# Kernel optimization log

Hardware: AMD Instinct MI355X
Metric: run time of the kernel (lower is better)

The kernel has to match this reference:

```python
import jax, jax.numpy as jnp
import numpy as np

DIM = 256
HEADS = 8
DIM_HEAD = 64
INNER = HEADS * DIM_HEAD
NUM_BANDS = 16          # hard-coded in __init__
MAX_FREQ = 16.0         # hard-coded in __init__
NORM_SCALE = 51.0       # hard-coded in __init__
RPE_DIM = (NUM_BANDS * 2 + 1) * 2  # 66


def fourier_encode(x, max_freq, num_bands):
    # x: [...] -> [..., 2*num_bands+1]  (sin bands, cos bands, raw)
    x = x[..., None]
    scales = jnp.linspace(1.0, max_freq / 2.0, num_bands, dtype=x.dtype)
    xs = x * scales * jnp.pi
    return jnp.concatenate([jnp.sin(xs), jnp.cos(xs), x], axis=-1)


def rpe_features(query_pos, key_pos):
    # delta[b,i,j] = key_pos[b,j] - query_pos[b,i]  -> [B,Nq,Nk,2]
    delta = key_pos[:, None, :, :] - query_pos[:, :, None, :]
    dx = delta[..., 0] / NORM_SCALE
    dy = delta[..., 1] / NORM_SCALE
    dx = dx / (1.0 + jnp.abs(dx))
    dy = dy / (1.0 + jnp.abs(dy))
    x_enc = fourier_encode(dx, MAX_FREQ, NUM_BANDS)
    y_enc = fourier_encode(dy, MAX_FREQ, NUM_BANDS)
    return jnp.concatenate([x_enc, y_enc], axis=-1)  # [B,Nq,Nk,RPE_DIM]


def setup_inputs() -> dict:
    key = jax.random.key(0)
    ks = jax.random.split(key, 8)
    B, N = 1, 512
    x = jax.random.normal(ks[0], (B, N, DIM), dtype=jnp.float32)
    positions = jax.random.uniform(ks[1], (B, N, 2), dtype=jnp.float32) * 512.0
    s = 0.02
    Wq = jax.random.normal(ks[2], (DIM, INNER), dtype=jnp.float32) * s
    Wk = jax.random.normal(ks[3], (DIM + RPE_DIM, INNER), dtype=jnp.float32) * s
    Wv = jax.random.normal(ks[4], (DIM, INNER), dtype=jnp.float32) * s
    Wo = jax.random.normal(ks[5], (INNER, DIM), dtype=jnp.float32) * s
    bo = jnp.zeros((DIM,), dtype=jnp.float32)
    return {"x": x, "positions": positions, "Wq": Wq, "Wk": Wk, "Wv": Wv, "Wo": Wo, "bo": bo}


def reference(x, positions, Wq, Wk, Wv, Wo, bo):
    B, N, D = x.shape
    H, d = HEADS, DIM_HEAD
    scale = d ** -0.5

    rpe = rpe_features(positions, positions)          # [B,N,N,R]
    q = (x @ Wq).reshape(B, N, H, d)                  # [B,N,H,d]
    v = (x @ Wv).reshape(B, N, H, d)

    # k_ij = W_k @ concat(x_j, rpe_ij); split Wk to avoid expanding x to [B,N,N,D]
    Wk_x, Wk_r = Wk[:D], Wk[D:]
    k_content = x @ Wk_x                               # [B,N,INNER] (key j part)
    k_rpe = jnp.einsum('bijr,re->bije', rpe, Wk_r)     # [B,N,N,INNER]
    k = (k_content[:, None, :, :] + k_rpe).reshape(B, N, N, H, d)

    scores = jnp.einsum('bihd,bijhd->bhij', q, k) * scale
    attn = jax.nn.softmax(scores, axis=-1)
    out = jnp.einsum('bhij,bjhd->bihd', attn, v).reshape(B, N, H * d)
    return out @ Wo + bo
```

## Files before the change

### kernel.cpp

```cpp
#include <hip/hip_runtime.h>
#include <math.h>

#define NQ      512
#define DMODEL  256
#define DINNER  512
#define NH      8
#define DHEAD   64
#define SCALE   0.125f
#define PI_F    3.14159265358979323846f

#define Q_OFF   0
#define KC_OFF  262144
#define V_OFF   524288
#define QW_OFF  786432
#define SC_OFF  1114112
#define IN_OFF  3211264

__global__ __launch_bounds__(256) void k_proj(
    const float* __restrict__ x, const float* __restrict__ Wq,
    const float* __restrict__ Wk, const float* __restrict__ Wv,
    float* __restrict__ ws)
{
    const int z = blockIdx.z;
    const float* W = (z == 0) ? Wq : (z == 1) ? Wk : Wv;
    float* out = ws + ((z == 0) ? Q_OFF : (z == 1) ? KC_OFF : V_OFF);

    __shared__ alignas(16) float Xs[32][68];
    __shared__ alignas(16) float Bs[32][64];

    const int tx = threadIdx.x, ty = threadIdx.y;
    const int tid = ty * 16 + tx;
    const int row0 = blockIdx.y * 64, col0 = blockIdx.x * 64;

    float acc[4][4] = {};

    for (int k0 = 0; k0 < DMODEL; k0 += 32) {
        {
            const int m = tid >> 2;
            const int kk0 = (tid & 3) * 8;
            const float* src = x + (row0 + m) * DMODEL + k0 + kk0;
            float4 a0 = *(const float4*)(src);
            float4 a1 = *(const float4*)(src + 4);
            Xs[kk0 + 0][m] = a0.x; Xs[kk0 + 1][m] = a0.y;
            Xs[kk0 + 2][m] = a0.z; Xs[kk0 + 3][m] = a0.w;
            Xs[kk0 + 4][m] = a1.x; Xs[kk0 + 5][m] = a1.y;
            Xs[kk0 + 6][m] = a1.z; Xs[kk0 + 7][m] = a1.w;
        }
        {
            const int kk = tid >> 3;
            const int n0 = (tid & 7) * 8;
            const float* src = W + (k0 + kk) * DINNER + col0 + n0;
            *(float4*)&Bs[kk][n0]     = *(const float4*)(src);
            *(float4*)&Bs[kk][n0 + 4] = *(const float4*)(src + 4);
        }
        __syncthreads();
        #pragma unroll
        for (int kk = 0; kk < 32; ++kk) {
            float4 a4 = *(const float4*)&Xs[kk][ty * 4];
            float4 b4 = *(const float4*)&Bs[kk][tx * 4];
            float a[4] = {a4.x, a4.y, a4.z, a4.w};
            float b[4] = {b4.x, b4.y, b4.z, b4.w};
            #pragma unroll
            for (int ia = 0; ia < 4; ++ia)
                #pragma unroll
                for (int ib = 0; ib < 4; ++ib)
                    acc[ia][ib] += a[ia] * b[ib];
        }
        __syncthreads();
    }
    #pragma unroll
    for (int ia = 0; ia < 4; ++ia) {
        float4 o = make_float4(acc[ia][0], acc[ia][1], acc[ia][2], acc[ia][3]);
        *(float4*)&out[(row0 + ty * 4 + ia) * DINNER + col0 + tx * 4] = o;
    }
}

__global__ __launch_bounds__(256) void k_qw(
    const float* __restrict__ Wk, float* __restrict__ ws)
{
    const float* q = ws + Q_OFF;
    float* qW = ws + QW_OFF;
    const int h  = blockIdx.x >> 4;
    const int i0 = (blockIdx.x & 15) * 32;

    __shared__ float WrT[64][67];
    __shared__ alignas(16) float Qs[32][68];
    const int tid = threadIdx.x;

    for (int idx = tid; idx < 66 * 64; idx += 256) {
        int r = idx >> 6, d = idx & 63;
        WrT[d][r] = Wk[(DMODEL + r) * DINNER + h * DHEAD + d];
    }
    for (int idx = tid; idx < 32 * 16; idx += 256) {
        int m = idx >> 4, dq = (idx & 15) * 4;
        *(float4*)&Qs[m][dq] = *(const float4*)&q[(i0 + m) * DINNER + h * DHEAD + dq];
    }
    __syncthreads();

    for (int idx = tid; idx < 32 * 66; idx += 256) {
        int m = idx / 66, r = idx - m * 66;
        float acc = 0.f;
        #pragma unroll
        for (int d0 = 0; d0 < 64; d0 += 4) {
            float4 qf = *(const float4*)&Qs[m][d0];
            acc += qf.x * WrT[d0 + 0][r] + qf.y * WrT[d0 + 1][r]
                 + qf.z * WrT[d0 + 2][r] + qf.w * WrT[d0 + 3][r];
        }
        int slot;
        if      (r < 16)  slot = r * 32 + 0 + h;
        else if (r < 32)  slot = (r - 16) * 32 + 8 + h;
        else if (r == 32) slot = 512 + h;
        else if (r < 49)  slot = (r - 33) * 32 + 16 + h;
        else if (r < 65)  slot = (r - 49) * 32 + 24 + h;
        else              slot = 520 + h;
        qW[(i0 + m) * 528 + slot] = acc * SCALE;
    }
}

__global__ __launch_bounds__(256) void k_content(float* __restrict__ ws)
{
    const float* q  = ws + Q_OFF;
    const float* kc = ws + KC_OFF;
    float* sc = ws + SC_OFF;
    const int h = blockIdx.z;
    const int i0 = blockIdx.y * 64, j0 = blockIdx.x * 64;

    __shared__ alignas(16) float Qs[64][68];
    __shared__ alignas(16) float Ks[64][68];
    const int tx = threadIdx.x, ty = threadIdx.y;
    const int tid = ty * 16 + tx;
    {
        const int m = tid >> 2;
        const int d0 = (tid & 3) * 16;
        const float* qs = q  + (i0 + m) * DINNER + h * DHEAD + d0;
        const float* ks = kc + (j0 + m) * DINNER + h * DHEAD + d0;
        #pragma unroll
        for (int l = 0; l < 16; ++l) {
            Qs[d0 + l][m] = qs[l];
            Ks[d0 + l][m] = ks[l];
        }
    }
    __syncthreads();
    float acc[4][4] = {};
    #pragma unroll 8
    for (int d = 0; d < 64; ++d) {
        float4 a4 = *(const float4*)&Qs[d][ty * 4];
        float4 b4 = *(const float4*)&Ks[d][tx * 4];
        float a[4] = {a4.x, a4.y, a4.z, a4.w};
        float b[4] = {b4.x, b4.y, b4.z, b4.w};
        #pragma unroll
        for (int ia = 0; ia < 4; ++ia)
            #pragma unroll
            for (int ib = 0; ib < 4; ++ib)
                acc[ia][ib] += a[ia] * b[ib];
    }
    #pragma unroll
    for (int ia = 0; ia < 4; ++ia) {
        float4 o = make_float4(acc[ia][0] * SCALE, acc[ia][1] * SCALE,
                               acc[ia][2] * SCALE, acc[ia][3] * SCALE);
        *(float4*)&sc[((h * NQ) + i0 + ty * 4 + ia) * NQ + j0 + tx * 4] = o;
    }
}

__global__ __launch_bounds__(256) void k_rpe_softmax(
    const float* __restrict__ pos, float* __restrict__ ws)
{
    const float* qW = ws + QW_OFF;
    float* sc = ws + SC_OFF;
    const int i = blockIdx.x;
    const int tid = threadIdx.x;

    __shared__ alignas(16) float qw[528];
    __shared__ float pbuf[8][512];
    __shared__ float red[8];

    for (int idx = tid; idx < 528; idx += 256) qw[idx] = qW[i * 528 + idx];
    __syncthreads();

    const float pxi = pos[i * 2 + 0];
    const float pyi = pos[i * 2 + 1];
    const float4* qw4 = (const float4*)qw;

    #pragma unroll
    for (int jj = 0; jj < 2; ++jj) {
        const int j = tid + jj * 256;
        float dxr = (pos[j * 2 + 0] - pxi) * (1.0f / 51.0f);
        float dyr = (pos[j * 2 + 1] - pyi) * (1.0f / 51.0f);
        float dx = dxr / (1.0f + fabsf(dxr));
        float dy = dyr / (1.0f + fabsf(dyr));

        float s[8];
        #pragma unroll
        for (int h = 0; h < 8; ++h) s[h] = sc[((h * NQ) + i) * NQ + j];

        float sx, cx, sy, cy, sxp, cxp, syp, cyp;
        __sincosf(dx * PI_F, &sx, &cx);
        __sincosf(dx * (PI_F * 7.0f / 15.0f), &sxp, &cxp);
        __sincosf(dy * PI_F, &sy, &cy);
        __sincosf(dy * (PI_F * 7.0f / 15.0f), &syp, &cyp);

        #pragma unroll
        for (int b = 0; b < 16; ++b) {
            float4 wsx0 = qw4[b * 8 + 0], wsx1 = qw4[b * 8 + 1];
            float4 wcx0 = qw4[b * 8 + 2], wcx1 = qw4[b * 8 + 3];
            float4 wsy0 = qw4[b * 8 + 4], wsy1 = qw4[b * 8 + 5];
            float4 wcy0 = qw4[b * 8 + 6], wcy1 = qw4[b * 8 + 7];
            s[0] += sx * wsx0.x + cx * wcx0.x + sy * wsy0.x + cy * wcy0.x;
            s[1] += sx * wsx0.y + cx * wcx0.y + sy * wsy0.y + cy * wcy0.y;
            s[2] += sx * wsx0.z + cx * wcx0.z + sy * wsy0.z + cy * wcy0.z;
            s[3] += sx * wsx0.w + cx * wcx0.w + sy * wsy0.w + cy * wcy0.w;
            s[4] += sx * wsx1.x + cx * wcx1.x + sy * wsy1.x + cy * wcy1.x;
            s[5] += sx * wsx1.y + cx * wcx1.y + sy * wsy1.y + cy * wcy1.y;
            s[6] += sx * wsx1.z + cx * wcx1.z + sy * wsy1.z + cy * wcy1.z;
            s[7] += sx * wsx1.w + cx * wcx1.w + sy * wsy1.w + cy * wcy1.w;
            float t;
            t = sx * cxp + cx * sxp; cx = cx * cxp - sx * sxp; sx = t;
            t = sy * cyp + cy * syp; cy = cy * cyp - sy * syp; sy = t;
        }
        {
            float4 wdx0 = qw4[128], wdx1 = qw4[129];
            float4 wdy0 = qw4[130], wdy1 = qw4[131];
            s[0] += dx * wdx0.x + dy * wdy0.x;
            s[1] += dx * wdx0.y + dy * wdy0.y;
            s[2] += dx * wdx0.z + dy * wdy0.z;
            s[3] += dx * wdx0.w + dy * wdy0.w;
            s[4] += dx * wdx1.x + dy * wdy1.x;
            s[5] += dx * wdx1.y + dy * wdy1.y;
            s[6] += dx * wdx1.z + dy * wdy1.z;
            s[7] += dx * wdx1.w + dy * wdy1.w;
        }
        #pragma unroll
        for (int h = 0; h < 8; ++h) pbuf[h][j] = s[h];
    }
    __syncthreads();

    const int wave = tid >> 6, lane = tid & 63;
    for (int h = wave * 2; h < wave * 2 + 2; ++h) {
        float m = -1e30f;
        for (int jj2 = lane; jj2 < 512; jj2 += 64) m = fmaxf(m, pbuf[h][jj2]);
        #pragma unroll
        for (int off = 32; off; off >>= 1) m = fmaxf(m, __shfl_xor(m, off));
        float sum = 0.f;
        for (int jj2 = lane; jj2 < 512; jj2 += 64) {
            float e = __expf(pbuf[h][jj2] - m);
            pbuf[h][jj2] = e;
            sum += e;
        }
        #pragma unroll
        for (int off = 32; off; off >>= 1) sum += __shfl_xor(sum, off);
        if (lane == 0) red[h] = 1.0f / sum;
    }
    __syncthreads();
    #pragma unroll
    for (int h = 0; h < 8; ++h) {
        const float inv = red[h];
        sc[((h * NQ) + i) * NQ + tid]       = pbuf[h][tid] * inv;
        sc[((h * NQ) + i) * NQ + tid + 256] = pbuf[h][tid + 256] * inv;
    }
}

__global__ __launch_bounds__(256) void k_av(float* __restrict__ ws)
{
    const float* attn = ws + SC_OFF;
    const float* v    = ws + V_OFF;
    float* inner      = ws + IN_OFF;
    const int h  = blockIdx.y;
    const int i0 = blockIdx.x * 32;

    __shared__ alignas(16) float As[32][36];
    __shared__ alignas(16) float Vs[32][64];
    const int tx = threadIdx.x, ty = threadIdx.y;
    const int tid = ty * 16 + tx;

    float acc[2][4] = {};
    for (int k0 = 0; k0 < NQ; k0 += 32) {
        {
            const int m = tid >> 3;
            const int kk0 = (tid & 7) * 4;
            float4 a4 = *(const float4*)&attn[((h * NQ) + i0 + m) * NQ + k0 + kk0];
            As[kk0 + 0][m] = a4.x; As[kk0 + 1][m] = a4.y;
            As[kk0 + 2][m] = a4.z; As[kk0 + 3][m] = a4.w;
        }
        {
            const int kk = tid >> 3;
            const int n0 = (tid & 7) * 8;
            const float* src = v + (k0 + kk) * DINNER + h * DHEAD + n0;
            *(float4*)&Vs[kk][n0]     = *(const float4*)(src);
            *(float4*)&Vs[kk][n0 + 4] = *(const float4*)(src + 4);
        }
        __syncthreads();
        #pragma unroll
        for (int kk = 0; kk < 32; ++kk) {
            float2 a2 = *(const float2*)&As[kk][ty * 2];
            float4 b4 = *(const float4*)&Vs[kk][tx * 4];
            float b[4] = {b4.x, b4.y, b4.z, b4.w};
            #pragma unroll
            for (int ib = 0; ib < 4; ++ib) {
                acc[0][ib] += a2.x * b[ib];
                acc[1][ib] += a2.y * b[ib];
            }
        }
        __syncthreads();
    }
    #pragma unroll
    for (int ia = 0; ia < 2; ++ia) {
        float4 o = make_float4(acc[ia][0], acc[ia][1], acc[ia][2], acc[ia][3]);
        *(float4*)&inner[(i0 + ty * 2 + ia) * DINNER + h * DHEAD + tx * 4] = o;
    }
}

__global__ __launch_bounds__(256) void k_out(
    const float* __restrict__ Wo, const float* __restrict__ bo,
    float* __restrict__ ws, float* __restrict__ outp)
{
    const float* inner = ws + IN_OFF;
    const int c0 = blockIdx.x * 32;
    const int i0 = blockIdx.y * 32;

    __shared__ alignas(16) float Xs[32][36];
    __shared__ alignas(16) float Bs[32][32];
    const int tx = threadIdx.x, ty = threadIdx.y;
    const int tid = ty * 16 + tx;

    float acc[2][2] = {};
    for (int k0 = 0; k0 < DINNER; k0 += 32) {
        {
            const int m = tid >> 3;
            const int kk0 = (tid & 7) * 4;
            float4 a4 = *(const float4*)&inner[(i0 + m) * DINNER + k0 + kk0];
            Xs[kk0 + 0][m] = a4.x; Xs[kk0 + 1][m] = a4.y;
            Xs[kk0 + 2][m] = a4.z; Xs[kk0 + 3][m] = a4.w;
        }
        {
            const int kk = tid >> 3;
            const int n0 = (tid & 7) * 4;
            *(float4*)&Bs[kk][n0] = *(const float4*)&Wo[(k0 + kk) * DMODEL + c0 + n0];
        }
        __syncthreads();
        #pragma unroll
        for (int kk = 0; kk < 32; ++kk) {
            float2 a2 = *(const float2*)&Xs[kk][ty * 2];
            float2 b2 = *(const float2*)&Bs[kk][tx * 2];
            acc[0][0] += a2.x * b2.x;
            acc[0][1] += a2.x * b2.y;
            acc[1][0] += a2.y * b2.x;
            acc[1][1] += a2.y * b2.y;
        }
        __syncthreads();
    }
    #pragma unroll
    for (int ia = 0; ia < 2; ++ia) {
        float2 o;
        o.x = acc[ia][0] + bo[c0 + tx * 2 + 0];
        o.y = acc[ia][1] + bo[c0 + tx * 2 + 1];
        *(float2*)&outp[(i0 + ty * 2 + ia) * DMODEL + c0 + tx * 2] = o;
    }
}

extern "C" void kernel_launch(void* const* d_in, const int* in_sizes, int n_in,
                              void* d_out, int out_size, void* d_ws, size_t ws_size,
                              hipStream_t stream)
{
    const float* x   = (const float*)d_in[0];
    const float* pos = (const float*)d_in[1];
    const float* Wq  = (const float*)d_in[2];
    const float* Wk  = (const float*)d_in[3];
    const float* Wv  = (const float*)d_in[4];
    const float* Wo  = (const float*)d_in[5];
    const float* bo  = (const float*)d_in[6];
    float* out = (float*)d_out;
    float* ws  = (float*)d_ws;

    k_proj<<<dim3(8, 8, 3), dim3(16, 16), 0, stream>>>(x, Wq, Wk, Wv, ws);
    k_qw<<<dim3(128), dim3(256), 0, stream>>>(Wk, ws);
    k_content<<<dim3(8, 8, 8), dim3(16, 16), 0, stream>>>(ws);
    k_rpe_softmax<<<dim3(512), dim3(256), 0, stream>>>(pos, ws);
    k_av<<<dim3(16, 8), dim3(16, 16), 0, stream>>>(ws);
    k_out<<<dim3(8, 16), dim3(16, 16), 0, stream>>>(Wo, bo, ws, out);
}
```

Baseline: 166.9 us.

## Fuse content scores, RPE bias, softmax and AV into flash-style attention kernel

```diff
diff --git a/kernel.cpp b/kernel.cpp
--- a/kernel.cpp
+++ b/kernel.cpp
@@ -13,8 +13,7 @@
 #define KC_OFF  262144
 #define V_OFF   524288
 #define QW_OFF  786432
-#define SC_OFF  1114112
-#define IN_OFF  3211264
+#define IN_OFF  1064960
 
 __global__ __launch_bounds__(256) void k_proj(
     const float* __restrict__ x, const float* __restrict__ Wq,
@@ -106,207 +105,173 @@
             acc += qf.x * WrT[d0 + 0][r] + qf.y * WrT[d0 + 1][r]
                  + qf.z * WrT[d0 + 2][r] + qf.w * WrT[d0 + 3][r];
         }
-        int slot;
-        if      (r < 16)  slot = r * 32 + 0 + h;
-        else if (r < 32)  slot = (r - 16) * 32 + 8 + h;
-        else if (r == 32) slot = 512 + h;
-        else if (r < 49)  slot = (r - 33) * 32 + 16 + h;
-        else if (r < 65)  slot = (r - 49) * 32 + 24 + h;
-        else              slot = 520 + h;
-        qW[(i0 + m) * 528 + slot] = acc * SCALE;
-    }
-}
-
-__global__ __launch_bounds__(256) void k_content(float* __restrict__ ws)
+        int p = (r < 32) ? r : (r == 32) ? 64 : (r < 65) ? (r - 1) : 65;
+        qW[(i0 + m) * 544 + h * 68 + p] = acc * SCALE;
+    }
+}
+
+__device__ __forceinline__ float rpe_eval(float2 pq, float2 pk, const float4* cw)
+{
+    float dxr = (pk.x - pq.x) * (1.0f / 51.0f);
+    float dyr = (pk.y - pq.y) * (1.0f / 51.0f);
+    float dx = dxr / (1.0f + fabsf(dxr));
+    float dy = dyr / (1.0f + fabsf(dyr));
+    float thx = dx * PI_F, dlx = dx * (PI_F * 7.0f / 15.0f);
+    float thy = dy * PI_F, dly = dy * (PI_F * 7.0f / 15.0f);
+    float sxa, cxa, sxb, cxb, sya, cya, syb, cyb;
+    __sincosf(thx, &sxa, &cxa);
+    __sincosf(thx + dlx, &sxb, &cxb);
+    __sincosf(thy, &sya, &cya);
+    __sincosf(thy + dly, &syb, &cyb);
+    const float Kx = 2.0f * __cosf(dlx);
+    const float Ky = 2.0f * __cosf(dly);
+    float acc = 0.f;
+    #pragma unroll
+    for (int g = 0; g < 4; ++g) {
+        float4 wsx = cw[g], wcx = cw[4 + g], wsy = cw[8 + g], wcy = cw[12 + g];
+        #pragma unroll
+        for (int k = 0; k < 4; ++k) {
+            float a = (&wsx.x)[k], b = (&wcx.x)[k], c = (&wsy.x)[k], e = (&wcy.x)[k];
+            acc += sxa * a + cxa * b + sya * c + cya * e;
+            float t;
+            t = Kx * sxb - sxa; sxa = sxb; sxb = t;
+            t = Kx * cxb - cxa; cxa = cxb; cxb = t;
+            t = Ky * syb - sya; sya = syb; syb = t;
+            t = Ky * cyb - cya; cya = cyb; cyb = t;
+        }
+    }
+    float4 tw = cw[16];
+    acc += dx * tw.x + dy * tw.y;
+    return acc;
+}
+
+__device__ __forceinline__ float wave_max(float v)
+{
+    #pragma unroll
+    for (int off = 32; off; off >>= 1) v = fmaxf(v, __shfl_xor(v, off));
+    return v;
+}
+__device__ __forceinline__ float wave_sum(float v)
+{
+    #pragma unroll
+    for (int off = 32; off; off >>= 1) v += __shfl_xor(v, off);
+    return v;
+}
+
+__global__ __launch_bounds__(256) void k_attn(
+    const float* __restrict__ pos, float* __restrict__ ws)
 {
     const float* q  = ws + Q_OFF;
     const float* kc = ws + KC_OFF;
-    float* sc = ws + SC_OFF;
-    const int h = blockIdx.z;
-    const int i0 = blockIdx.y * 64, j0 = blockIdx.x * 64;
-
-    __shared__ alignas(16) float Qs[64][68];
+    const float* v  = ws + V_OFF;
+    const float* qW = ws + QW_OFF;
+    float* inner    = ws + IN_OFF;
+
+    const int h  = blockIdx.x >> 6;
+    const int i0 = (blockIdx.x & 63) * 8;
+    const int tid = threadIdx.x;
+    const int w = tid >> 6, l = tid & 63;
+    const int iw = w * 2;
+
+    __shared__ alignas(16) float Qs[64][12];
+    __shared__ alignas(16) float qWs[8][68];
+    __shared__ float2 posQs[8];
     __shared__ alignas(16) float Ks[64][68];
-    const int tx = threadIdx.x, ty = threadIdx.y;
-    const int tid = ty * 16 + tx;
-    {
-        const int m = tid >> 2;
-        const int d0 = (tid & 3) * 16;
-        const float* qs = q  + (i0 + m) * DINNER + h * DHEAD + d0;
-        const float* ks = kc + (j0 + m) * DINNER + h * DHEAD + d0;
-        #pragma unroll
-        for (int l = 0; l < 16; ++l) {
-            Qs[d0 + l][m] = qs[l];
-            Ks[d0 + l][m] = ks[l];
-        }
-    }
-    __syncthreads();
-    float acc[4][4] = {};
-    #pragma unroll 8
-    for (int d = 0; d < 64; ++d) {
-        float4 a4 = *(const float4*)&Qs[d][ty * 4];
-        float4 b4 = *(const float4*)&Ks[d][tx * 4];
-        float a[4] = {a4.x, a4.y, a4.z, a4.w};
-        float b[4] = {b4.x, b4.y, b4.z, b4.w};
-        #pragma unroll
-        for (int ia = 0; ia < 4; ++ia)
-            #pragma unroll
-            for (int ib = 0; ib < 4; ++ib)
-                acc[ia][ib] += a[ia] * b[ib];
-    }
-    #pragma unroll
-    for (int ia = 0; ia < 4; ++ia) {
-        float4 o = make_float4(acc[ia][0] * SCALE, acc[ia][1] * SCALE,
-                               acc[ia][2] * SCALE, acc[ia][3] * SCALE);
-        *(float4*)&sc[((h * NQ) + i0 + ty * 4 + ia) * NQ + j0 + tx * 4] = o;
-    }
-}
-
-__global__ __launch_bounds__(256) void k_rpe_softmax(
-    const float* __restrict__ pos, float* __restrict__ ws)
-{
-    const float* qW = ws + QW_OFF;
-    float* sc = ws + SC_OFF;
-    const int i = blockIdx.x;
-    const int tid = threadIdx.x;
-
-    __shared__ alignas(16) float qw[528];
-    __shared__ float pbuf[8][512];
-    __shared__ float red[8];
-
-    for (int idx = tid; idx < 528; idx += 256) qw[idx] = qW[i * 528 + idx];
-    __syncthreads();
-
-    const float pxi = pos[i * 2 + 0];
-    const float pyi = pos[i * 2 + 1];
-    const float4* qw4 = (const float4*)qw;
-
-    #pragma unroll
-    for (int jj = 0; jj < 2; ++jj) {
-        const int j = tid + jj * 256;
-        float dxr = (pos[j * 2 + 0] - pxi) * (1.0f / 51.0f);
-        float dyr = (pos[j * 2 + 1] - pyi) * (1.0f / 51.0f);
-        float dx = dxr / (1.0f + fabsf(dxr));
-        float dy = dyr / (1.0f + fabsf(dyr));
-
-        float s[8];
-        #pragma unroll
-        for (int h = 0; h < 8; ++h) s[h] = sc[((h * NQ) + i) * NQ + j];
-
-        float sx, cx, sy, cy, sxp, cxp, syp, cyp;
-        __sincosf(dx * PI_F, &sx, &cx);
-        __sincosf(dx * (PI_F * 7.0f / 15.0f), &sxp, &cxp);
-        __sincosf(dy * PI_F, &sy, &cy);
-        __sincosf(dy * (PI_F * 7.0f / 15.0f), &syp, &cyp);
-
-        #pragma unroll
-        for (int b = 0; b < 16; ++b) {
-            float4 wsx0 = qw4[b * 8 + 0], wsx1 = qw4[b * 8 + 1];
-            float4 wcx0 = qw4[b * 8 + 2], wcx1 = qw4[b * 8 + 3];
-            float4 wsy0 = qw4[b * 8 + 4], wsy1 = qw4[b * 8 + 5];
-            float4 wcy0 = qw4[b * 8 + 6], wcy1 = qw4[b * 8 + 7];
-            s[0] += sx * wsx0.x + cx * wcx0.x + sy * wsy0.x + cy * wcy0.x;
-            s[1] += sx * wsx0.y + cx * wcx0.y + sy * wsy0.y + cy * wcy0.y;
-            s[2] += sx * wsx0.z + cx * wcx0.z + sy * wsy0.z + cy * wcy0.z;
-            s[3] += sx * wsx0.w + cx * wcx0.w + sy * wsy0.w + cy * wcy0.w;
-            s[4] += sx * wsx1.x + cx * wcx1.x + sy * wsy1.x + cy * wcy1.x;
-            s[5] += sx * wsx1.y + cx * wcx1.y + sy * wsy1.y + cy * wcy1.y;
-            s[6] += sx * wsx1.z + cx * wcx1.z + sy * wsy1.z + cy * wcy1.z;
-            s[7] += sx * wsx1.w + cx * wcx1.w + sy * wsy1.w + cy * wcy1.w;
-            float t;
-            t = sx * cxp + cx * sxp; cx = cx * cxp - sx * sxp; sx = t;
-            t = sy * cyp + cy * syp; cy = cy * cyp - sy * syp; sy = t;
-        }
-        {
-            float4 wdx0 = qw4[128], wdx1 = qw4[129];
-            float4 wdy0 = qw4[130], wdy1 = qw4[131];
-            s[0] += dx * wdx0.x + dy * wdy0.x;
-            s[1] += dx * wdx0.y + dy * wdy0.y;
-            s[2] += dx * wdx0.z + dy * wdy0.z;
-            s[3] += dx * wdx0.w + dy * wdy0.w;
-            s[4] += dx * wdx1.x + dy * wdy1.x;
-            s[5] += dx * wdx1.y + dy * wdy1.y;
-            s[6] += dx * wdx1.z + dy * wdy1.z;
-            s[7] += dx * wdx1.w + dy * wdy1.w;
-        }
-        #pragma unroll
-        for (int h = 0; h < 8; ++h) pbuf[h][j] = s[h];
-    }
-    __syncthreads();
-
-    const int wave = tid >> 6, lane = tid & 63;
-    for (int h = wave * 2; h < wave * 2 + 2; ++h) {
-        float m = -1e30f;
-        for (int jj2 = lane; jj2 < 512; jj2 += 64) m = fmaxf(m, pbuf[h][jj2]);
-        #pragma unroll
-        for (int off = 32; off; off >>= 1) m = fmaxf(m, __shfl_xor(m, off));
-        float sum = 0.f;
-        for (int jj2 = lane; jj2 < 512; jj2 += 64) {
-            float e = __expf(pbuf[h][jj2] - m);
-            pbuf[h][jj2] = e;
-            sum += e;
-        }
-        #pragma unroll
-        for (int off = 32; off; off >>= 1) sum += __shfl_xor(sum, off);
-        if (lane == 0) red[h] = 1.0f / sum;
-    }
-    __syncthreads();
-    #pragma unroll
-    for (int h = 0; h < 8; ++h) {
-        const float inv = red[h];
-        sc[((h * NQ) + i) * NQ + tid]       = pbuf[h][tid] * inv;
-        sc[((h * NQ) + i) * NQ + tid + 256] = pbuf[h][tid + 256] * inv;
-    }
-}
-
-__global__ __launch_bounds__(256) void k_av(float* __restrict__ ws)
-{
-    const float* attn = ws + SC_OFF;
-    const float* v    = ws + V_OFF;
-    float* inner      = ws + IN_OFF;
-    const int h  = blockIdx.y;
-    const int i0 = blockIdx.x * 32;
-
-    __shared__ alignas(16) float As[32][36];
-    __shared__ alignas(16) float Vs[32][64];
-    const int tx = threadIdx.x, ty = threadIdx.y;
-    const int tid = ty * 16 + tx;
-
-    float acc[2][4] = {};
-    for (int k0 = 0; k0 < NQ; k0 += 32) {
-        {
-            const int m = tid >> 3;
-            const int kk0 = (tid & 7) * 4;
-            float4 a4 = *(const float4*)&attn[((h * NQ) + i0 + m) * NQ + k0 + kk0];
-            As[kk0 + 0][m] = a4.x; As[kk0 + 1][m] = a4.y;
-            As[kk0 + 2][m] = a4.z; As[kk0 + 3][m] = a4.w;
-        }
-        {
-            const int kk = tid >> 3;
-            const int n0 = (tid & 7) * 8;
-            const float* src = v + (k0 + kk) * DINNER + h * DHEAD + n0;
-            *(float4*)&Vs[kk][n0]     = *(const float4*)(src);
-            *(float4*)&Vs[kk][n0 + 4] = *(const float4*)(src + 4);
-        }
-        __syncthreads();
-        #pragma unroll
-        for (int kk = 0; kk < 32; ++kk) {
-            float2 a2 = *(const float2*)&As[kk][ty * 2];
-            float4 b4 = *(const float4*)&Vs[kk][tx * 4];
-            float b[4] = {b4.x, b4.y, b4.z, b4.w};
-            #pragma unroll
-            for (int ib = 0; ib < 4; ++ib) {
-                acc[0][ib] += a2.x * b[ib];
-                acc[1][ib] += a2.y * b[ib];
-            }
-        }
-        __syncthreads();
-    }
-    #pragma unroll
-    for (int ia = 0; ia < 2; ++ia) {
-        float4 o = make_float4(acc[ia][0], acc[ia][1], acc[ia][2], acc[ia][3]);
-        *(float4*)&inner[(i0 + ty * 2 + ia) * DINNER + h * DHEAD + tx * 4] = o;
-    }
+    __shared__ alignas(16) float Vs[64][68];
+    __shared__ float2 posKs[64];
+    __shared__ alignas(16) float Ps[8][68];
+
+    if (tid < 128) {
+        int m = tid >> 4, d4 = (tid & 15) * 4;
+        float4 qv = *(const float4*)&q[(i0 + m) * DINNER + h * DHEAD + d4];
+        Qs[d4 + 0][m] = qv.x; Qs[d4 + 1][m] = qv.y;
+        Qs[d4 + 2][m] = qv.z; Qs[d4 + 3][m] = qv.w;
+    }
+    for (int idx = tid; idx < 8 * 68; idx += 256) {
+        int m = idx / 68, c = idx - m * 68;
+        qWs[m][c] = qW[(i0 + m) * 544 + h * 68 + c];
+    }
+    if (tid < 8) posQs[tid] = *(const float2*)&pos[(i0 + tid) * 2];
+
+    float m0 = -1e30f, m1 = -1e30f;
+    float ls0 = 0.f, ls1 = 0.f;
+    float acc0 = 0.f, acc1 = 0.f;
+
+    const float4* cw0 = (const float4*)&qWs[iw][0];
+    const float4* cw1 = (const float4*)&qWs[iw + 1][0];
+
+    for (int jt = 0; jt < 8; ++jt) {
+        const int j0 = jt * 64;
+        __syncthreads();
+        {
+            const int jj = tid >> 2, dg = (tid & 3) * 16;
+            const float* sk = kc + (j0 + jj) * DINNER + h * DHEAD + dg;
+            float4 a = *(const float4*)(sk),     b = *(const float4*)(sk + 4),
+                   c = *(const float4*)(sk + 8), d = *(const float4*)(sk + 12);
+            Ks[dg +  0][jj] = a.x; Ks[dg +  1][jj] = a.y; Ks[dg +  2][jj] = a.z; Ks[dg +  3][jj] = a.w;
+            Ks[dg +  4][jj] = b.x; Ks[dg +  5][jj] = b.y; Ks[dg +  6][jj] = b.z; Ks[dg +  7][jj] = b.w;
+            Ks[dg +  8][jj] = c.x; Ks[dg +  9][jj] = c.y; Ks[dg + 10][jj] = c.z; Ks[dg + 11][jj] = c.w;
+            Ks[dg + 12][jj] = d.x; Ks[dg + 13][jj] = d.y; Ks[dg + 14][jj] = d.z; Ks[dg + 15][jj] = d.w;
+            const float* sv = v + (j0 + jj) * DINNER + h * DHEAD + dg;
+            *(float4*)&Vs[jj][dg +  0] = *(const float4*)(sv);
+            *(float4*)&Vs[jj][dg +  4] = *(const float4*)(sv + 4);
+            *(float4*)&Vs[jj][dg +  8] = *(const float4*)(sv + 8);
+            *(float4*)&Vs[jj][dg + 12] = *(const float4*)(sv + 12);
+            if (tid < 64) posKs[tid] = *(const float2*)&pos[(j0 + tid) * 2];
+        }
+        __syncthreads();
+
+        float s0 = 0.f, s1 = 0.f;
+        #pragma unroll 8
+        for (int d = 0; d < 64; ++d) {
+            float kf = Ks[d][l];
+            float2 q2 = *(const float2*)&Qs[d][iw];
+            s0 += q2.x * kf;
+            s1 += q2.y * kf;
+        }
+        s0 *= SCALE; s1 *= SCALE;
+
+        float2 pk = posKs[l];
+        s0 += rpe_eval(posQs[iw],     pk, cw0);
+        s1 += rpe_eval(posQs[iw + 1], pk, cw1);
+
+        {
+            float mt = wave_max(s0);
+            float mn = fmaxf(m0, mt);
+            float rs = __expf(m0 - mn);
+            float p  = __expf(s0 - mn);
+            ls0 = ls0 * rs + wave_sum(p);
+            acc0 *= rs;
+            m0 = mn;
+            Ps[iw][l] = p;
+        }
+        {
+            float mt = wave_max(s1);
+            float mn = fmaxf(m1, mt);
+            float rs = __expf(m1 - mn);
+            float p  = __expf(s1 - mn);
+            ls1 = ls1 * rs + wave_sum(p);
+            acc1 *= rs;
+            m1 = mn;
+            Ps[iw + 1][l] = p;
+        }
+        __syncthreads();
+
+        #pragma unroll
+        for (int jg = 0; jg < 16; ++jg) {
+            float4 p0 = *(const float4*)&Ps[iw][jg * 4];
+            float4 p1 = *(const float4*)&Ps[iw + 1][jg * 4];
+            float v0 = Vs[jg * 4 + 0][l];
+            float v1 = Vs[jg * 4 + 1][l];
+            float v2 = Vs[jg * 4 + 2][l];
+            float v3 = Vs[jg * 4 + 3][l];
+            acc0 += p0.x * v0 + p0.y * v1 + p0.z * v2 + p0.w * v3;
+            acc1 += p1.x * v0 + p1.y * v1 + p1.z * v2 + p1.w * v3;
+        }
+    }
+
+    inner[(i0 + iw)     * DINNER + h * DHEAD + l] = acc0 / ls0;
+    inner[(i0 + iw + 1) * DINNER + h * DHEAD + l] = acc1 / ls1;
 }
 
 __global__ __launch_bounds__(256) void k_out(
@@ -373,8 +338,6 @@
 
     k_proj<<<dim3(8, 8, 3), dim3(16, 16), 0, stream>>>(x, Wq, Wk, Wv, ws);
     k_qw<<<dim3(128), dim3(256), 0, stream>>>(Wk, ws);
-    k_content<<<dim3(8, 8, 8), dim3(16, 16), 0, stream>>>(ws);
-    k_rpe_softmax<<<dim3(512), dim3(256), 0, stream>>>(pos, ws);
-    k_av<<<dim3(16, 8), dim3(16, 16), 0, stream>>>(ws);
+    k_attn<<<dim3(512), dim3(256), 0, stream>>>(pos, ws);
     k_out<<<dim3(8, 16), dim3(16, 16), 0, stream>>>(Wo, bo, ws, out);
 }
```

After: 155.6 us. 6.8% less time.
